# Optimization experiments

Measured on AMD Instinct MI355X. Metric: run time of the kernel, lower is better.

## Reference

```python
import jax, jax.numpy as jnp
import numpy as np

DEGREE = 8  # selected_degree for every neuron (== max_degree)


def cheb_features(x):
    """x: [B, D] in [-1, 1]. Returns [B, D*(DEGREE+1)] with per-dim
    Chebyshev T_0..T_DEGREE contiguous (matches torch stack-then-cat layout)."""
    B, D = x.shape
    Ts = [jnp.ones_like(x), x]
    for _ in range(DEGREE - 1):
        Ts.append(2.0 * x * Ts[-1] - Ts[-2])  # shared recurrence T_{k+1}=2xT_k-T_{k-1}
    T = jnp.stack(Ts[: DEGREE + 1], axis=-1)  # [B, D, DEGREE+1]
    return T.reshape(B, D * (DEGREE + 1))


def setup_inputs() -> dict:
    key = jax.random.key(0)
    k1, k2 = jax.random.split(key, 2)
    B, D, N = 32768, 256, 256
    F = D * (DEGREE + 1)  # 2304
    x = jax.random.normal(k1, (B, D), dtype=jnp.float32)
    coeffs = jax.random.normal(k2, (N, F), dtype=jnp.float32) / np.float32(np.sqrt(F))
    hweights = jnp.ones((N,), dtype=jnp.float32)
    return {"x": x, "coeffs": coeffs, "hweights": hweights}


def reference(x, coeffs, hweights):
    # tanh squashes inputs into [-1, 1], the Chebyshev domain
    X = cheb_features(jnp.tanh(x))            # [B, F]
    per_neuron = X @ coeffs.T                 # [B, N] : transform @ coefficients per neuron
    return (per_neuron * hweights).sum(axis=1)  # stack over neurons then sum -> [B]
```

## Files before the change

### kernel.cpp

```cpp
#include <hip/hip_runtime.h>

#define B_ROWS 32768
#define D_DIM  256
#define N_NEUR 256
#define DEG    8
#define F_FEAT (D_DIM * (DEG + 1))

__global__ __launch_bounds__(256) void reduce_w_kernel(
    const float* __restrict__ coeffs, const float* __restrict__ h,
    float* __restrict__ w) {
  int f  = blockIdx.x * 256 + threadIdx.x;
  int n0 = blockIdx.y * 16;
  float acc = 0.f;
#pragma unroll
  for (int j = 0; j < 16; ++j) {
    int n = n0 + j;
    acc = fmaf(coeffs[(size_t)n * F_FEAT + f], h[n], acc);
  }
  atomicAdd(&w[f], acc);
}

__global__ __launch_bounds__(256) void kan_main_kernel(
    const float* __restrict__ x, const float* __restrict__ w,
    float* __restrict__ out) {
  const int lane = threadIdx.x & 63;

  float wreg[36];
  const float4* w4 = (const float4*)w;
#pragma unroll
  for (int q = 0; q < 9; ++q) {
    float4 v = w4[9 * lane + q];
    wreg[4 * q + 0] = v.x;
    wreg[4 * q + 1] = v.y;
    wreg[4 * q + 2] = v.z;
    wreg[4 * q + 3] = v.w;
  }

  int gw = (int)((blockIdx.x * blockDim.x + threadIdx.x) >> 6);
  int nw = (int)((gridDim.x * blockDim.x) >> 6);

  for (int row = gw; row < B_ROWS; row += nw) {
    const float4* xr = (const float4*)(x + (size_t)row * D_DIM);
    float4 xv = xr[lane];
    float xa[4] = {xv.x, xv.y, xv.z, xv.w};
    float acc = 0.f;
#pragma unroll
    for (int i = 0; i < 4; ++i) {
      float e = __expf(xa[i] + xa[i]);
      float r = __builtin_amdgcn_rcpf(e + 1.f);
      float t = fmaf(-2.f, r, 1.f);
      float t2 = t + t;
      const float* wd = &wreg[9 * i];
      float s    = fmaf(t, wd[1], wd[0]);
      float tkm1 = 1.f, tk = t;
#pragma unroll
      for (int k = 2; k <= DEG; ++k) {
        float tn = fmaf(t2, tk, -tkm1);
        s  = fmaf(tn, wd[k], s);
        tkm1 = tk;
        tk   = tn;
      }
      acc += s;
    }
#pragma unroll
    for (int off = 32; off > 0; off >>= 1)
      acc += __shfl_down(acc, off, 64);
    if (lane == 0) out[row] = acc;
  }
}

extern "C" void kernel_launch(void* const* d_in, const int* in_sizes, int n_in,
                              void* d_out, int out_size, void* d_ws, size_t ws_size,
                              hipStream_t stream) {
  const float* x      = (const float*)d_in[0];
  const float* coeffs = (const float*)d_in[1];
  const float* h      = (const float*)d_in[2];
  float* out = (float*)d_out;
  float* w   = (float*)d_ws;

  hipMemsetAsync(w, 0, F_FEAT * sizeof(float), stream);
  reduce_w_kernel<<<dim3(F_FEAT / 256, N_NEUR / 16), 256, 0, stream>>>(coeffs, h, w);
  kan_main_kernel<<<2048, 256, 0, stream>>>(x, w, out);
}
```

Baseline: 83.73 us.

## Drop memset and atomics in weight reduction; batch four rows per wavefront

The coefficient reduction now runs in one 1024-thread block per 256 features. Each wavefront sums 16 neurons with float4 loads, and the partials are combined in shared memory, which removes the memset launch and the global atomics. The main kernel now processes four rows per wavefront with all x loads issued up front. A combined shuffle reduction then writes four outputs at once. The cost is that the reduction uses only 9 blocks, and the main kernel relies on the grid exactly covering B (2048*4 waves*4 rows = 32768).

```diff
diff --git a/kernel.cpp b/kernel.cpp
--- a/kernel.cpp
+++ b/kernel.cpp
@@ -5,19 +5,40 @@
 #define N_NEUR 256
 #define DEG    8
 #define F_FEAT (D_DIM * (DEG + 1))
+#define F4     (F_FEAT / 4)
 
-__global__ __launch_bounds__(256) void reduce_w_kernel(
+__global__ __launch_bounds__(1024) void reduce_w_kernel(
     const float* __restrict__ coeffs, const float* __restrict__ h,
     float* __restrict__ w) {
-  int f  = blockIdx.x * 256 + threadIdx.x;
-  int n0 = blockIdx.y * 16;
-  float acc = 0.f;
+  __shared__ float4 part[16][64];
+  const int lane = threadIdx.x & 63;
+  const int wv   = threadIdx.x >> 6;
+  const float4* c4 = (const float4*)coeffs;
+  const int f4 = blockIdx.x * 64 + lane;
+
+  float4 a = make_float4(0.f, 0.f, 0.f, 0.f);
 #pragma unroll
   for (int j = 0; j < 16; ++j) {
-    int n = n0 + j;
-    acc = fmaf(coeffs[(size_t)n * F_FEAT + f], h[n], acc);
+    int n = wv * 16 + j;
+    float hn = h[n];
+    float4 c = c4[(size_t)n * F4 + f4];
+    a.x = fmaf(c.x, hn, a.x);
+    a.y = fmaf(c.y, hn, a.y);
+    a.z = fmaf(c.z, hn, a.z);
+    a.w = fmaf(c.w, hn, a.w);
   }
-  atomicAdd(&w[f], acc);
+  part[wv][lane] = a;
+  __syncthreads();
+
+  if (threadIdx.x < 64) {
+    float4 s = part[0][lane];
+#pragma unroll
+    for (int q = 1; q < 16; ++q) {
+      float4 p = part[q][lane];
+      s.x += p.x; s.y += p.y; s.z += p.z; s.w += p.w;
+    }
+    ((float4*)w)[f4] = s;
+  }
 }
 
 __global__ __launch_bounds__(256) void kan_main_kernel(
@@ -36,37 +57,51 @@
     wreg[4 * q + 3] = v.w;
   }
 
-  int gw = (int)((blockIdx.x * blockDim.x + threadIdx.x) >> 6);
-  int nw = (int)((gridDim.x * blockDim.x) >> 6);
+  const int gw = (int)((blockIdx.x * blockDim.x + threadIdx.x) >> 6);
+  const int r0 = gw * 4;
 
-  for (int row = gw; row < B_ROWS; row += nw) {
-    const float4* xr = (const float4*)(x + (size_t)row * D_DIM);
-    float4 xv = xr[lane];
-    float xa[4] = {xv.x, xv.y, xv.z, xv.w};
-    float acc = 0.f;
+  const float4* xr = (const float4*)(x + (size_t)r0 * D_DIM);
+  float4 xv[4];
+#pragma unroll
+  for (int r = 0; r < 4; ++r) xv[r] = xr[r * 64 + lane];
+
+  float acc[4];
+#pragma unroll
+  for (int r = 0; r < 4; ++r) {
+    float xa[4] = {xv[r].x, xv[r].y, xv[r].z, xv[r].w};
+    float s4 = 0.f;
 #pragma unroll
     for (int i = 0; i < 4; ++i) {
-      float e = __expf(xa[i] + xa[i]);
-      float r = __builtin_amdgcn_rcpf(e + 1.f);
-      float t = fmaf(-2.f, r, 1.f);
-      float t2 = t + t;
+      float e   = __expf(xa[i] + xa[i]);
+      float rcp = __builtin_amdgcn_rcpf(e + 1.f);
+      float t   = fmaf(-2.f, rcp, 1.f);
+      float t2  = t + t;
       const float* wd = &wreg[9 * i];
       float s    = fmaf(t, wd[1], wd[0]);
       float tkm1 = 1.f, tk = t;
 #pragma unroll
       for (int k = 2; k <= DEG; ++k) {
         float tn = fmaf(t2, tk, -tkm1);
-        s  = fmaf(tn, wd[k], s);
+        s    = fmaf(tn, wd[k], s);
         tkm1 = tk;
         tk   = tn;
       }
-      acc += s;
+      s4 += s;
     }
+    acc[r] = s4;
+  }
+
 #pragma unroll
-    for (int off = 32; off > 0; off >>= 1)
-      acc += __shfl_down(acc, off, 64);
-    if (lane == 0) out[row] = acc;
+  for (int r = 0; r < 4; ++r) {
+    acc[r] += __shfl_xor(acc[r], 32, 64);
+    acc[r] += __shfl_xor(acc[r], 16, 64);
   }
+  float v = (lane < 32) ? ((lane < 16) ? acc[0] : acc[1])
+                        : ((lane < 48) ? acc[2] : acc[3]);
+#pragma unroll
+  for (int off = 8; off; off >>= 1) v += __shfl_xor(v, off, 64);
+
+  if ((lane & 15) == 0) out[r0 + (lane >> 4)] = v;
 }
 
 extern "C" void kernel_launch(void* const* d_in, const int* in_sizes, int n_in,
@@ -78,7 +113,6 @@
   float* out = (float*)d_out;
   float* w   = (float*)d_ws;
 
-  hipMemsetAsync(w, 0, F_FEAT * sizeof(float), stream);
-  reduce_w_kernel<<<dim3(F_FEAT / 256, N_NEUR / 16), 256, 0, stream>>>(coeffs, h, w);
+  reduce_w_kernel<<<9, 1024, 0, stream>>>(coeffs, h, w);
   kan_main_kernel<<<2048, 256, 0, stream>>>(x, w, out);
 }
```

New measurement: 81.67 us. -2.5%, faster.
